# Kernel optimization log

Hardware: AMD Instinct MI355X
Metric: run time of the kernel (lower is better)

Reference implementation:

```python
import jax, jax.numpy as jnp
import numpy as np

TOP_K = 2  # config.moe_config['moe_top_k']


def setup_inputs() -> dict:
    key = jax.random.key(0)
    k1, k2, k3, k4 = jax.random.split(key, 4)
    B, S, H, F, E = 2, 1024, 1024, 2048, 8
    def init(k, shape, fan_in):
        return jax.random.normal(k, shape, jnp.float32) / np.float32(np.sqrt(fan_in))
    return {
        "hidden_states": jax.random.normal(k1, (B, S, H), jnp.float32),
        "router_w": init(k2, (H, E), H),          # Linear(hidden, E, bias=False)
        "W1": init(k3, (E, H, 2 * F), H),          # per-expert Linear(hidden, 2*ffn)
        "W2": init(k4, (E, F, H), F),              # per-expert Linear(ffn, hidden)
    }


def reference(hidden_states, router_w, W1, W2):
    B, S, H = hidden_states.shape
    E = router_w.shape[1]
    x = hidden_states.reshape(-1, H)                      # [N, H], N = B*S
    N = x.shape[0]

    # router: logits -> fp32 softmax -> top-k -> renormalize (matches torch)
    logits = x @ router_w                                  # [N, E]
    probs = jax.nn.softmax(logits.astype(jnp.float32), axis=-1)
    rw, sel = jax.lax.top_k(probs, TOP_K)                  # [N, k]
    rw = rw / rw.sum(axis=-1, keepdims=True)
    rw = rw.astype(x.dtype)

    # combine weights per (token, expert); top-k experts are distinct so add==set
    cw = jnp.zeros((N, E), x.dtype).at[jnp.arange(N)[:, None], sel].add(rw)

    # per-expert SwiGLU MLP over all tokens, masked combine (full-capacity MoE)
    h = jnp.einsum('nh,ehf->enf', x, W1)                   # [E, N, 2F]
    a, b = jnp.split(h, 2, axis=-1)                        # gate, value halves
    g = jax.nn.silu(a) * b                                 # [E, N, F]
    y = jnp.einsum('enf,efh->enh', g, W2)                  # [E, N, H]
    out = jnp.einsum('enh,ne->nh', y, cw)                  # weighted scatter-combine
    return out.reshape(B, S, H)
```

## Files before the change

kernel.cpp:

```cpp
#include <hip/hip_runtime.h>
#include <hip/hip_bf16.h>

#define H_DIM 1024
#define E_NUM 8
#define F_DIM 2048
#define N_TOK 2048
typedef unsigned int uint;
typedef short bf16x8 __attribute__((ext_vector_type(8)));
typedef float f32x4 __attribute__((ext_vector_type(4)));

#define WS_CNT   0
#define WS_LIST  256
#define WS_W     (WS_LIST + 8*N_TOK*4)
#define WS_G     131072
#define WS_Y     (WS_G + 4096*2048*2)
#define WS_XB    WS_Y


static __device__ __forceinline__ uint f2bf(float f) {
    uint u = __builtin_bit_cast(uint, f);
    return (u + 0x7FFFu + ((u >> 16) & 1u)) >> 16;
}
static __device__ __forceinline__ float bflo(uint u) { return __builtin_bit_cast(float, u << 16); }
static __device__ __forceinline__ float bfhi(uint u) { return __builtin_bit_cast(float, u & 0xFFFF0000u); }
static __device__ __forceinline__ uint cvtpk(float a, float b) {
    uint r;
    asm("v_cvt_pk_bf16_f32 %0, %1, %2" : "=v"(r) : "v"(a), "v"(b));
    return r;
}
static __device__ __forceinline__ void gload_lds16(const void* g, void* l) {
    __builtin_amdgcn_global_load_lds(
        (const __attribute__((address_space(1))) unsigned int*)g,
        (__attribute__((address_space(3))) unsigned int*)l,
        16, 0, 0);
}
template<int N> static __device__ __forceinline__ void vmwait() {
    if constexpr (N == 0)      asm volatile("s_waitcnt vmcnt(0)" ::: "memory");
    else if constexpr (N == 4) asm volatile("s_waitcnt vmcnt(4)" ::: "memory");
    else if constexpr (N == 8) asm volatile("s_waitcnt vmcnt(8)" ::: "memory");
}

__global__ __launch_bounds__(256) void cvt_x_kernel(const float* __restrict__ x,
                                                    unsigned short* __restrict__ xb)
{
    int c = blockIdx.x * 256 + threadIdx.x;
    int row = c >> 7, b = c & 127;
    int t = b >> 3, s = b & 7;
    int klo = t*64 + (s >> 2)*32 + (s & 3)*4;
    const float* xr = x + (size_t)row * H_DIM;
    float4 lo = *(const float4*)(xr + klo);
    float4 hi = *(const float4*)(xr + klo + 16);
    uint4 o;
    o.x = cvtpk(lo.x, lo.y); o.y = cvtpk(lo.z, lo.w);
    o.z = cvtpk(hi.x, hi.y); o.w = cvtpk(hi.z, hi.w);
    *(uint4*)(xb + (size_t)row * H_DIM + b*8) = o;
}

__global__ __launch_bounds__(256) void router_kernel(
    const float* __restrict__ x, const float* __restrict__ rw,
    int* __restrict__ cnt, int* __restrict__ list, float* __restrict__ w_entry)
{
    int wave = threadIdx.x >> 6, lane = threadIdx.x & 63;
    int n = blockIdx.x * 4 + wave;
    const float* xr = x + (size_t)n * H_DIM;
    float acc[8] = {0,0,0,0,0,0,0,0};
    #pragma unroll
    for (int i = 0; i < H_DIM/64; ++i) {
        int h = i*64 + lane;
        float xv = xr[h];
        const float4* rr = (const float4*)(rw + (size_t)h*8);
        float4 r0 = rr[0], r1 = rr[1];
        acc[0] += xv*r0.x; acc[1] += xv*r0.y; acc[2] += xv*r0.z; acc[3] += xv*r0.w;
        acc[4] += xv*r1.x; acc[5] += xv*r1.y; acc[6] += xv*r1.z; acc[7] += xv*r1.w;
    }
    #pragma unroll
    for (int e = 0; e < 8; ++e) {
        float v = acc[e];
        #pragma unroll
        for (int off = 32; off; off >>= 1) v += __shfl_xor(v, off);
        acc[e] = v;
    }
    int e0 = 0;
    #pragma unroll
    for (int e = 1; e < 8; ++e) if (acc[e] > acc[e0]) e0 = e;
    int e1 = -1;
    #pragma unroll
    for (int e = 0; e < 8; ++e) if (e != e0 && (e1 < 0 || acc[e] > acc[e1])) e1 = e;
    float w0 = 1.0f / (1.0f + __expf(acc[e1] - acc[e0]));
    float w1 = 1.0f - w0;
    if (lane == 0) {
        int p0 = atomicAdd(&cnt[e0], 1);
        list[e0*N_TOK + p0] = n*2;
        w_entry[n*2] = w0;
        int p1 = atomicAdd(&cnt[e1], 1);
        list[e1*N_TOK + p1] = n*2 + 1;
        w_entry[n*2+1] = w1;
    }
}

template<int IS_G1>
__global__ __launch_bounds__(256, 2) void moe_gemm_kernel(
    const unsigned short* __restrict__ Asrc, const float* __restrict__ W,
    const int* __restrict__ cnt, const int* __restrict__ list,
    const float* __restrict__ w_entry, unsigned short* __restrict__ dst)
{
    constexpr int KTOT  = IS_G1 ? H_DIM : F_DIM;
    constexpr int BLD   = IS_G1 ? 2*F_DIM : H_DIM;
    constexpr int DLD   = IS_G1 ? F_DIM : H_DIM;
    constexpr int ALD   = IS_G1 ? H_DIM : F_DIM;
    constexpr int ROWS  = 128;
    constexpr int NM    = 8;
    constexpr int NA    = 4;
    constexpr int NMT   = 16;
    constexpr int NNT   = IS_G1 ? 32 : 8;
    constexpr int NT    = KTOT / 32;

    __shared__ __align__(16) unsigned short As[2][ROWS*64];
    __shared__ __align__(16) uint Bs[2][32*128];

    constexpr int nb = NMT * NNT * E_NUM;
    constexpr int chunk = nb >> 3;
    int bid = blockIdx.x;
    int f  = (bid & 7) * chunk + (bid >> 3);
    int mt = f % NMT;
    int nt = (f / NMT) % NNT;
    int e  = f / (NMT * NNT);

    const int c = cnt[e];
    if (mt * ROWS >= c) return;
    const int tid = threadIdx.x;
    const int lane = tid & 63, wid = tid >> 6;
    const int l15 = lane & 15, lg = lane >> 4;
    const int lbase = e * N_TOK + mt * ROWS;

    const unsigned short* a_src[NA];
    #pragma unroll
    for (int i = 0; i < NA; ++i) {
        int sl  = wid*(NA*1024) + i*1024 + lane*16;
        int row = sl >> 7;
        int kb  = ((sl >> 4) & 7) ^ (row & 7);
        int rr  = (mt*ROWS + row) < c ? row : (c - 1 - mt*ROWS);
        int ent = list[lbase + rr];
        int arow = IS_G1 ? (ent >> 1) : ent;
        a_src[i] = Asrc + (size_t)arow * ALD + kb*8;
    }

    const float* Wb = W + (size_t)e * (size_t)(IS_G1 ? H_DIM*2*F_DIM : F_DIM*H_DIM);
    const float* b_srcp[4];
    #pragma unroll
    for (int i = 0; i < 4; ++i) {
        int k  = wid*8 + i*2 + (lane >> 5);
        int c4 = (lane & 31) ^ (k & 12);
        int gc;
        if constexpr (IS_G1) gc = (c4 < 16) ? (nt*64 + 4*c4) : (F_DIM + nt*64 + 4*(c4-16));
        else                 gc = nt*128 + 4*c4;
        b_srcp[i] = Wb + (size_t)k * BLD + gc;
    }

    int a_addr[NM][2];
    #pragma unroll
    for (int m = 0; m < NM; ++m)
        #pragma unroll
        for (int p = 0; p < 2; ++p) {
            int row = m*16 + l15;
            a_addr[m][p] = row*128 + ((p*64 + lg*16) ^ ((row & 7) << 4));
        }
    int b_base[2];
    #pragma unroll
    for (int j = 0; j < 2; ++j) {
        int cb = IS_G1 ? (j ? (4 + wid) : wid) : (wid*2 + j);
        b_base[j] = ((cb*16 + l15) * 4) ^ (lg << 6);
    }

    f32x4 acc[NM][2];
    #pragma unroll
    for (int m = 0; m < NM; ++m)
        #pragma unroll
        for (int j = 0; j < 2; ++j) acc[m][j] = (f32x4){0.f,0.f,0.f,0.f};

    auto STAGE_A = [&](int s) {
        #pragma unroll
        for (int i = 0; i < NA; ++i)
            gload_lds16(a_src[i] + s*64, (char*)As[s & 1] + wid*(NA*1024) + i*1024);
    };
    auto STAGE_B = [&](int t) {
        #pragma unroll
        for (int i = 0; i < 4; ++i)
            gload_lds16(b_srcp[i] + (size_t)t * 32 * BLD, (char*)Bs[t & 1] + wid*4096 + i*1024);
    };
    auto compute = [&](int P, int abuf) {
        const char* ab  = (const char*)As[abuf];
        const char* bb0 = (const char*)Bs[P];
        bf16x8 bfr[2];
        #pragma unroll
        for (int j = 0; j < 2; ++j) {
            const char* bb = bb0 + (4*lg)*512 + b_base[j];
            float fA0 = *(const float*)(bb);
            float fA1 = *(const float*)(bb + 512);
            float fA2 = *(const float*)(bb + 1024);
            float fA3 = *(const float*)(bb + 1536);
            float fB0 = *(const float*)(bb + 8192);
            float fB1 = *(const float*)(bb + 8192 + 512);
            float fB2 = *(const float*)(bb + 8192 + 1024);
            float fB3 = *(const float*)(bb + 8192 + 1536);
            union { uint u[4]; bf16x8 v; } bu;
            bu.u[0] = cvtpk(fA0, fA1);
            bu.u[1] = cvtpk(fA2, fA3);
            bu.u[2] = cvtpk(fB0, fB1);
            bu.u[3] = cvtpk(fB2, fB3);
            bfr[j] = bu.v;
        }
        #pragma unroll
        for (int m = 0; m < NM; ++m) {
            bf16x8 af = *(const bf16x8*)(ab + (P ? a_addr[m][1] : a_addr[m][0]));
            #pragma unroll
            for (int j = 0; j < 2; ++j)
                acc[m][j] = __builtin_amdgcn_mfma_f32_16x16x32_bf16(af, bfr[j], acc[m][j], 0, 0, 0);
        }
    };

    STAGE_A(0); STAGE_B(0); STAGE_B(1);

    for (int tp = 0; tp < NT/2 - 1; ++tp) {
        const int t = 2*tp, ab = tp & 1;
        vmwait<4>();
        __builtin_amdgcn_sched_barrier(0);
        __builtin_amdgcn_s_barrier();
        asm volatile("" ::: "memory");
        compute(0, ab);
        asm volatile("" ::: "memory");
        __builtin_amdgcn_s_barrier();
        asm volatile("" ::: "memory");
        STAGE_A(tp + 1);
        STAGE_B(t + 2);
        vmwait<8>();
        __builtin_amdgcn_sched_barrier(0);
        __builtin_amdgcn_s_barrier();
        asm volatile("" ::: "memory");
        compute(1, ab);
        asm volatile("" ::: "memory");
        __builtin_amdgcn_s_barrier();
        asm volatile("" ::: "memory");
        STAGE_B(t + 3);
    }
    {
        const int ab = (NT/2 - 1) & 1;
        vmwait<4>();
        __builtin_amdgcn_sched_barrier(0);
        __builtin_amdgcn_s_barrier();
        asm volatile("" ::: "memory");
        compute(0, ab);
        asm volatile("" ::: "memory");
        vmwait<0>();
        __builtin_amdgcn_sched_barrier(0);
        __builtin_amdgcn_s_barrier();
        asm volatile("" ::: "memory");
        compute(1, ab);
    }

    if constexpr (IS_G1) {
        __syncthreads();
        unsigned short (*tb)[64] = (unsigned short (*)[64])As;
        const int pcol = ((wid >> 1)*4 + (l15 >> 2))*8 + (wid & 1)*4 + (l15 & 3);
        #pragma unroll
        for (int m = 0; m < NM; ++m) {
            f32x4 ga = acc[m][0], gv = acc[m][1];
            #pragma unroll
            for (int i = 0; i < 4; ++i) {
                int row = m*16 + lg*4 + i;
                float a = ga[i];
                tb[row][pcol] = (unsigned short)f2bf((a / (1.f + __expf(-a))) * gv[i]);
            }
        }
        __syncthreads();
        int r = tid >> 1, half = tid & 1;
        if (mt*ROWS + r < c) {
            int ent = list[lbase + r];
            char* dp = (char*)dst + ((size_t)ent * DLD + nt*64)*2 + half*64;
            const char* sp = (const char*)&tb[r][0] + half*64;
            #pragma unroll
            for (int q = 0; q < 4; ++q)
                *(uint4*)(dp + q*16) = *(const uint4*)(sp + q*16);
        }
    } else {
        float (*tb)[128] = (float (*)[128])Bs;
        #pragma unroll
        for (int h = 0; h < 4; ++h) {
            __syncthreads();
            #pragma unroll
            for (int mm = 0; mm < 2; ++mm) {
                int m = h*2 + mm;
                #pragma unroll
                for (int j = 0; j < 2; ++j)
                    #pragma unroll
                    for (int i = 0; i < 4; ++i) {
                        int row = mm*16 + lg*4 + i;
                        tb[row][(wid*2 + j)*16 + l15] = acc[m][j][i];
                    }
            }
            __syncthreads();
            int r = tid >> 3, ch = tid & 7;
            int rg = h*32 + r;
            if (mt*ROWS + rg < c) {
                int ent = list[lbase + rg];
                float w = w_entry[ent];
                const float* src = &tb[r][ch*16];
                uint4 o0, o1;
                o0.x = cvtpk(w*src[0],  w*src[1]);  o0.y = cvtpk(w*src[2],  w*src[3]);
                o0.z = cvtpk(w*src[4],  w*src[5]);  o0.w = cvtpk(w*src[6],  w*src[7]);
                o1.x = cvtpk(w*src[8],  w*src[9]);  o1.y = cvtpk(w*src[10], w*src[11]);
                o1.z = cvtpk(w*src[12], w*src[13]); o1.w = cvtpk(w*src[14], w*src[15]);
                char* dp = (char*)dst + ((size_t)ent * DLD + nt*128 + ch*16)*2;
                *(uint4*)(dp)      = o0;
                *(uint4*)(dp + 16) = o1;
            }
        }
    }
}

__global__ __launch_bounds__(256) void combine_kernel(
    const unsigned short* __restrict__ y, float* __restrict__ out)
{
    int gid = blockIdx.x * 256 + threadIdx.x;
    size_t base = (size_t)gid * 8;
    int n = (int)(base >> 10), h = (int)(base & 1023);
    const uint4 a = *(const uint4*)(y + (size_t)(2*n)   * 1024 + h);
    const uint4 b = *(const uint4*)(y + (size_t)(2*n+1) * 1024 + h);
    float4 o0, o1;
    o0.x = bflo(a.x)+bflo(b.x); o0.y = bfhi(a.x)+bfhi(b.x);
    o0.z = bflo(a.y)+bflo(b.y); o0.w = bfhi(a.y)+bfhi(b.y);
    o1.x = bflo(a.z)+bflo(b.z); o1.y = bfhi(a.z)+bfhi(b.z);
    o1.z = bflo(a.w)+bflo(b.w); o1.w = bfhi(a.w)+bfhi(b.w);
    *(float4*)(out + base)     = o0;
    *(float4*)(out + base + 4) = o1;
}

extern "C" void kernel_launch(void* const* d_in, const int* in_sizes, int n_in,
                              void* d_out, int out_size, void* d_ws, size_t ws_size,
                              hipStream_t stream) {
    const float* x  = (const float*)d_in[0];
    const float* rw = (const float*)d_in[1];
    const float* W1 = (const float*)d_in[2];
    const float* W2 = (const float*)d_in[3];
    float* out = (float*)d_out;
    char* ws = (char*)d_ws;
    int*   cnt     = (int*)(ws + WS_CNT);
    int*   list    = (int*)(ws + WS_LIST);
    float* w_entry = (float*)(ws + WS_W);
    unsigned short* g  = (unsigned short*)(ws + WS_G);
    unsigned short* y  = (unsigned short*)(ws + WS_Y);
    unsigned short* xb = (unsigned short*)(ws + WS_XB);

    hipMemsetAsync(cnt, 0, E_NUM * sizeof(int), stream);
    cvt_x_kernel<<<N_TOK*H_DIM/2048, 256, 0, stream>>>(x, xb);
    router_kernel<<<N_TOK/4, 256, 0, stream>>>(x, rw, cnt, list, w_entry);
    moe_gemm_kernel<1><<<16*32*E_NUM, 256, 0, stream>>>(xb, W1, cnt, list, w_entry, g);
    moe_gemm_kernel<0><<<16*8*E_NUM, 256, 0, stream>>>(g,  W2, cnt, list, w_entry, y);
    combine_kernel<<<(out_size/8 + 255)/256, 256, 0, stream>>>(y, out);
}
```

Measured before the change: 225.9 us.

## Convert B weights to bf16 in registers before LDS and deepen A pipeline

The fp32 expert weights are now loaded into registers with plain global loads, packed to bf16 in pairs along K, and written to LDS, instead of being copied to LDS as fp32 via direct-to-LDS loads and converted on every read. This halves the LDS footprint and LDS read traffic for B and removes repeated conversions inside the MFMA loop. The A tiles gain a four-deep buffer and the loop is restructured into a register-prefetched software pipeline with explicit vmcnt and lgkmcnt waits. The cost is more VGPR pressure from holding prefetched B quads and extra LDS writes and barriers per step, which may hurt occupancy at two blocks per CU.

New measurement: 222.7 us. No clear change (-1.4%).

```diff
diff --git a/kernel.cpp b/kernel.cpp
--- a/kernel.cpp
+++ b/kernel.cpp
@@ -35,9 +35,15 @@
         16, 0, 0);
 }
 template<int N> static __device__ __forceinline__ void vmwait() {
-    if constexpr (N == 0)      asm volatile("s_waitcnt vmcnt(0)" ::: "memory");
-    else if constexpr (N == 4) asm volatile("s_waitcnt vmcnt(4)" ::: "memory");
-    else if constexpr (N == 8) asm volatile("s_waitcnt vmcnt(8)" ::: "memory");
+    if constexpr (N == 0)       asm volatile("s_waitcnt vmcnt(0)" ::: "memory");
+    else if constexpr (N == 4)  asm volatile("s_waitcnt vmcnt(4)" ::: "memory");
+    else if constexpr (N == 12) asm volatile("s_waitcnt vmcnt(12)" ::: "memory");
+    else if constexpr (N == 16) asm volatile("s_waitcnt vmcnt(16)" ::: "memory");
+}
+static __device__ __forceinline__ void lgk0_bar() {
+    asm volatile("s_waitcnt lgkmcnt(0)" ::: "memory");
+    __builtin_amdgcn_s_barrier();
+    asm volatile("" ::: "memory");
 }
 
 __global__ __launch_bounds__(256) void cvt_x_kernel(const float* __restrict__ x,
@@ -113,10 +119,10 @@
     constexpr int NA    = 4;
     constexpr int NMT   = 16;
     constexpr int NNT   = IS_G1 ? 32 : 8;
-    constexpr int NT    = KTOT / 32;
-
-    __shared__ __align__(16) unsigned short As[2][ROWS*64];
-    __shared__ __align__(16) uint Bs[2][32*128];
+    constexpr int NP    = KTOT / 64;
+
+    __shared__ __align__(16) unsigned short As[4][ROWS*64];
+    __shared__ __align__(16) uint Bs[2][16*128];
 
     constexpr int nb = NMT * NNT * E_NUM;
     constexpr int chunk = nb >> 3;
@@ -146,15 +152,16 @@
     }
 
     const float* Wb = W + (size_t)e * (size_t)(IS_G1 ? H_DIM*2*F_DIM : F_DIM*H_DIM);
-    const float* b_srcp[4];
-    #pragma unroll
-    for (int i = 0; i < 4; ++i) {
-        int k  = wid*8 + i*2 + (lane >> 5);
-        int c4 = (lane & 31) ^ (k & 12);
+    const float* b_src[2]; int b_dst[2];
+    #pragma unroll
+    for (int s = 0; s < 2; ++s) {
+        int q = tid + s*256;
+        int kp = q >> 5, c4 = q & 31;
         int gc;
         if constexpr (IS_G1) gc = (c4 < 16) ? (nt*64 + 4*c4) : (F_DIM + nt*64 + 4*(c4-16));
         else                 gc = nt*128 + 4*c4;
-        b_srcp[i] = Wb + (size_t)k * BLD + gc;
+        b_src[s] = Wb + (size_t)(2*kp) * BLD + gc;
+        b_dst[s] = (kp*512 + c4*16) ^ ((kp & 4) << 4);
     }
 
     int a_addr[NM][2];
@@ -166,10 +173,11 @@
             a_addr[m][p] = row*128 + ((p*64 + lg*16) ^ ((row & 7) << 4));
         }
     int b_base[2];
+    const int xorv = ((2*lg) & 4) << 4;
     #pragma unroll
     for (int j = 0; j < 2; ++j) {
         int cb = IS_G1 ? (j ? (4 + wid) : wid) : (wid*2 + j);
-        b_base[j] = ((cb*16 + l15) * 4) ^ (lg << 6);
+        b_base[j] = (2*lg)*512 + (((cb*16 + l15) * 4) ^ xorv);
     }
 
     f32x4 acc[NM][2];
@@ -178,36 +186,43 @@
         #pragma unroll
         for (int j = 0; j < 2; ++j) acc[m][j] = (f32x4){0.f,0.f,0.f,0.f};
 
+    struct BQ { float4 a0, a1, b0, b1; };
+    auto loadB = [&](int t) {
+        BQ q;
+        const float* p0 = b_src[0] + (size_t)t * 32 * BLD;
+        q.a0 = *(const float4*)p0;
+        q.a1 = *(const float4*)(p0 + BLD);
+        const float* p1 = b_src[1] + (size_t)t * 32 * BLD;
+        q.b0 = *(const float4*)p1;
+        q.b1 = *(const float4*)(p1 + BLD);
+        return q;
+    };
+    auto dswB = [&](const BQ& q, int buf) {
+        uint4 w0, w1;
+        w0.x = cvtpk(q.a0.x, q.a1.x); w0.y = cvtpk(q.a0.y, q.a1.y);
+        w0.z = cvtpk(q.a0.z, q.a1.z); w0.w = cvtpk(q.a0.w, q.a1.w);
+        w1.x = cvtpk(q.b0.x, q.b1.x); w1.y = cvtpk(q.b0.y, q.b1.y);
+        w1.z = cvtpk(q.b0.z, q.b1.z); w1.w = cvtpk(q.b0.w, q.b1.w);
+        *(uint4*)((char*)Bs[buf] + b_dst[0]) = w0;
+        *(uint4*)((char*)Bs[buf] + b_dst[1]) = w1;
+    };
     auto STAGE_A = [&](int s) {
         #pragma unroll
         for (int i = 0; i < NA; ++i)
-            gload_lds16(a_src[i] + s*64, (char*)As[s & 1] + wid*(NA*1024) + i*1024);
-    };
-    auto STAGE_B = [&](int t) {
-        #pragma unroll
-        for (int i = 0; i < 4; ++i)
-            gload_lds16(b_srcp[i] + (size_t)t * 32 * BLD, (char*)Bs[t & 1] + wid*4096 + i*1024);
+            gload_lds16(a_src[i] + s*64, (char*)As[s & 3] + wid*(NA*1024) + i*1024);
     };
     auto compute = [&](int P, int abuf) {
-        const char* ab  = (const char*)As[abuf];
+        const char* ab  = (const char*)As + abuf*(ROWS*128);
         const char* bb0 = (const char*)Bs[P];
         bf16x8 bfr[2];
         #pragma unroll
         for (int j = 0; j < 2; ++j) {
-            const char* bb = bb0 + (4*lg)*512 + b_base[j];
-            float fA0 = *(const float*)(bb);
-            float fA1 = *(const float*)(bb + 512);
-            float fA2 = *(const float*)(bb + 1024);
-            float fA3 = *(const float*)(bb + 1536);
-            float fB0 = *(const float*)(bb + 8192);
-            float fB1 = *(const float*)(bb + 8192 + 512);
-            float fB2 = *(const float*)(bb + 8192 + 1024);
-            float fB3 = *(const float*)(bb + 8192 + 1536);
+            const char* bb = bb0 + b_base[j];
             union { uint u[4]; bf16x8 v; } bu;
-            bu.u[0] = cvtpk(fA0, fA1);
-            bu.u[1] = cvtpk(fA2, fA3);
-            bu.u[2] = cvtpk(fB0, fB1);
-            bu.u[3] = cvtpk(fB2, fB3);
+            bu.u[0] = *(const uint*)(bb);
+            bu.u[1] = *(const uint*)(bb + 512);
+            bu.u[2] = *(const uint*)(bb + 8*512);
+            bu.u[3] = *(const uint*)(bb + 9*512);
             bfr[j] = bu.v;
         }
         #pragma unroll
@@ -219,43 +234,55 @@
         }
     };
 
-    STAGE_A(0); STAGE_B(0); STAGE_B(1);
-
-    for (int tp = 0; tp < NT/2 - 1; ++tp) {
-        const int t = 2*tp, ab = tp & 1;
-        vmwait<4>();
-        __builtin_amdgcn_sched_barrier(0);
-        __builtin_amdgcn_s_barrier();
-        asm volatile("" ::: "memory");
-        compute(0, ab);
-        asm volatile("" ::: "memory");
-        __builtin_amdgcn_s_barrier();
-        asm volatile("" ::: "memory");
-        STAGE_A(tp + 1);
-        STAGE_B(t + 2);
-        vmwait<8>();
-        __builtin_amdgcn_sched_barrier(0);
-        __builtin_amdgcn_s_barrier();
-        asm volatile("" ::: "memory");
-        compute(1, ab);
-        asm volatile("" ::: "memory");
-        __builtin_amdgcn_s_barrier();
-        asm volatile("" ::: "memory");
-        STAGE_B(t + 3);
+    STAGE_A(0);
+    BQ q0 = loadB(0);
+    BQ q1 = loadB(1);
+    STAGE_A(1);
+    BQ q2 = loadB(2);
+    BQ q3 = loadB(3);
+
+    for (int tp = 0; tp < NP - 2; tp += 2) {
+        const int t = 2*tp;
+        vmwait<16>(); __builtin_amdgcn_sched_barrier(0);
+        dswB(q0, 0);
+        lgk0_bar();
+        STAGE_A(tp + 2);
+        compute(0, tp & 3);
+        vmwait<16>(); __builtin_amdgcn_sched_barrier(0);
+        dswB(q1, 1);
+        lgk0_bar();
+        q0 = loadB(t + 4);
+        q1 = loadB(t + 5);
+        compute(1, tp & 3);
+        vmwait<16>(); __builtin_amdgcn_sched_barrier(0);
+        dswB(q2, 0);
+        lgk0_bar();
+        STAGE_A(tp + 3);
+        compute(0, (tp + 1) & 3);
+        vmwait<16>(); __builtin_amdgcn_sched_barrier(0);
+        dswB(q3, 1);
+        lgk0_bar();
+        q2 = loadB(t + 6);
+        q3 = loadB(t + 7);
+        compute(1, (tp + 1) & 3);
     }
     {
-        const int ab = (NT/2 - 1) & 1;
-        vmwait<4>();
-        __builtin_amdgcn_sched_barrier(0);
-        __builtin_amdgcn_s_barrier();
-        asm volatile("" ::: "memory");
-        compute(0, ab);
-        asm volatile("" ::: "memory");
-        vmwait<0>();
-        __builtin_amdgcn_sched_barrier(0);
-        __builtin_amdgcn_s_barrier();
-        asm volatile("" ::: "memory");
-        compute(1, ab);
+        vmwait<16>(); __builtin_amdgcn_sched_barrier(0);
+        dswB(q0, 0);
+        lgk0_bar();
+        compute(0, (NP - 2) & 3);
+        vmwait<12>(); __builtin_amdgcn_sched_barrier(0);
+        dswB(q1, 1);
+        lgk0_bar();
+        compute(1, (NP - 2) & 3);
+        vmwait<4>(); __builtin_amdgcn_sched_barrier(0);
+        dswB(q2, 0);
+        lgk0_bar();
+        compute(0, (NP - 1) & 3);
+        vmwait<0>(); __builtin_amdgcn_sched_barrier(0);
+        dswB(q3, 1);
+        lgk0_bar();
+        compute(1, (NP - 1) & 3);
     }
 
     if constexpr (IS_G1) {
@@ -279,11 +306,11 @@
             char* dp = (char*)dst + ((size_t)ent * DLD + nt*64)*2 + half*64;
             const char* sp = (const char*)&tb[r][0] + half*64;
             #pragma unroll
-            for (int q = 0; q < 4; ++q)
-                *(uint4*)(dp + q*16) = *(const uint4*)(sp + q*16);
+            for (int qq = 0; qq < 4; ++qq)
+                *(uint4*)(dp + qq*16) = *(const uint4*)(sp + qq*16);
         }
     } else {
-        float (*tb)[128] = (float (*)[128])Bs;
+        float (*tb)[128] = (float (*)[128])As;
         #pragma unroll
         for (int h = 0; h < 4; ++h) {
             __syncthreads();
```
